# Kernel optimization log

Hardware: AMD Instinct MI355X
Metric: run time of the kernel (lower is better)

## Reference

```python
import jax, jax.numpy as jnp
import numpy as np

N_NODES = 20000
N_EDGES = 150000
FEAT = 64
HEADS = 8
N_RBF = 20
CUTOFF = 5.0


def painn_rbf(dist):
    # PaiNN radial basis used in NFF: sin(n*pi*d/cutoff)/d, n = 1..n_rbf
    n = jnp.arange(1, N_RBF + 1, dtype=dist.dtype)  # [n_rbf]
    d = dist[:, None]  # [E, 1]
    return jnp.sin(n * jnp.pi * d / CUTOFF) / d  # [E, n_rbf]


def cosine_envelope(dist):
    # 0.5 * (cos(pi*d/cutoff) + 1), zero beyond cutoff
    env = 0.5 * (jnp.cos(jnp.pi * dist / CUTOFF) + 1.0)
    return jnp.where(dist < CUTOFF, env, 0.0)


def setup_inputs() -> dict:
    key = jax.random.key(0)
    ks = jax.random.split(key, 7)
    dist = jax.random.uniform(ks[0], (N_EDGES,), minval=0.5, maxval=CUTOFF, dtype=jnp.float32)
    nbrs = jax.random.randint(ks[1], (N_EDGES, 2), 0, N_NODES, dtype=jnp.int64 if jax.config.jax_enable_x64 else jnp.int32)
    x_i = jax.random.normal(ks[2], (N_NODES, FEAT), dtype=jnp.float32)
    sf = np.float32(1.0 / np.sqrt(FEAT))
    sr = np.float32(1.0 / np.sqrt(N_RBF))
    W_q = jax.random.normal(ks[3], (HEADS, FEAT, FEAT), dtype=jnp.float32) * sf
    b_q = jnp.zeros((HEADS, FEAT), dtype=jnp.float32)
    W_k = jax.random.normal(ks[4], (HEADS, FEAT, FEAT), dtype=jnp.float32) * sf
    b_k = jnp.zeros((HEADS, FEAT), dtype=jnp.float32)
    W_dk = jax.random.normal(ks[5], (HEADS, FEAT, N_RBF), dtype=jnp.float32) * sr
    b_dk = jnp.zeros((HEADS, FEAT), dtype=jnp.float32)
    return {"dist": dist, "nbrs": nbrs, "x_i": x_i,
            "W_q": W_q, "b_q": b_q, "W_k": W_k, "b_k": b_k,
            "W_dk": W_dk, "b_dk": b_dk}


def reference(dist, nbrs, x_i, W_q, b_q, W_k, b_k, W_dk, b_dk):
    swish = jax.nn.silu
    xi = x_i[nbrs[:, 0]]  # [E, F]
    xj = x_i[nbrs[:, 1]]  # [E, F]
    edge_feats = painn_rbf(dist) * cosine_envelope(dist)[:, None]  # [E, n_rbf]
    # grouped Conv1d (kernel_size=1, groups=heads) == per-head linear
    query = jnp.einsum('ef,hgf->ehg', xi, W_q) + b_q  # [E, H, F]
    key = jnp.einsum('ef,hgf->ehg', xj, W_k) + b_k    # [E, H, F]
    d_k = swish(jnp.einsum('er,hfr->ehf', edge_feats, W_dk) + b_dk)  # [E, H, F]
    weights = swish(jnp.sum(query * key * d_k, axis=-1))  # [E, H]
    return weights
```

## Files before the change

### kernel.cpp

```cpp
#include <hip/hip_runtime.h>

#define N_NODES 20000
#define N_EDGES 150000
#define FEAT 64
#define HEADS 8
#define N_RBF 20
#define COLS 1024

typedef __attribute__((ext_vector_type(8))) short short8;
typedef __attribute__((ext_vector_type(4))) float f32x4;

union frag_u { int4 i; short8 s; };

__device__ __forceinline__ unsigned short f2bf(float x) {
    unsigned int u = __float_as_uint(x);
    unsigned int r = (u + 0x7FFFu + ((u >> 16) & 1u)) >> 16;
    return (unsigned short)r;
}
__device__ __forceinline__ unsigned int pack2bf(float lo, float hi) {
    return f2bf(lo) | ((unsigned int)f2bf(hi) << 16);
}
__device__ __forceinline__ float fsilu(float x) {
    return x * __builtin_amdgcn_rcpf(1.0f + __expf(-x));
}

__global__ __launch_bounds__(256, 4) void qk_project_mfma(
    const float* __restrict__ x,
    const float* __restrict__ Wq, const float* __restrict__ bq,
    const float* __restrict__ Wk, const float* __restrict__ bk,
    unsigned short* __restrict__ qk)
{
    const int tid = threadIdx.x;
    const int lane = tid & 63;
    const int wv = tid >> 6;
    const int l15 = lane & 15;
    const int g = lane >> 4;

    const int colBase = blockIdx.x * 256 + wv * 64;
    const bool isK = colBase >= 512;
    const float* W = isK ? Wk : Wq;
    const float* bias = isK ? bk : bq;
    const int colW = colBase & 511;

    short8 aw[4][2];
#pragma unroll
    for (int c = 0; c < 4; ++c) {
#pragma unroll
        for (int s = 0; s < 2; ++s) {
            const float* p = W + (colW + 16 * c + l15) * 64 + 32 * s + 8 * g;
            float4 v0 = *reinterpret_cast<const float4*>(p);
            float4 v1 = *reinterpret_cast<const float4*>(p + 4);
            frag_u f;
            f.i.x = pack2bf(v0.x, v0.y);
            f.i.y = pack2bf(v0.z, v0.w);
            f.i.z = pack2bf(v1.x, v1.y);
            f.i.w = pack2bf(v1.z, v1.w);
            aw[c][s] = f.s;
        }
    }
    float4 b4[4];
#pragma unroll
    for (int c = 0; c < 4; ++c)
        b4[c] = *reinterpret_cast<const float4*>(bias + colW + 16 * c + 4 * g);

    for (int i = 0; i < 8; ++i) {
        int nt = blockIdx.y * 8 + i;
        if (nt >= N_NODES / 16) break;
        int nodeBase = nt * 16;

        short8 bx[2];
#pragma unroll
        for (int s = 0; s < 2; ++s) {
            const float* p = x + (nodeBase + l15) * 64 + 32 * s + 8 * g;
            float4 v0 = *reinterpret_cast<const float4*>(p);
            float4 v1 = *reinterpret_cast<const float4*>(p + 4);
            frag_u f;
            f.i.x = pack2bf(v0.x, v0.y);
            f.i.y = pack2bf(v0.z, v0.w);
            f.i.z = pack2bf(v1.x, v1.y);
            f.i.w = pack2bf(v1.z, v1.w);
            bx[s] = f.s;
        }

#pragma unroll
        for (int c = 0; c < 4; ++c) {
            f32x4 acc = {0.f, 0.f, 0.f, 0.f};
#pragma unroll
            for (int s = 0; s < 2; ++s)
                acc = __builtin_amdgcn_mfma_f32_16x16x32_bf16(aw[c][s], bx[s], acc, 0, 0, 0);
            ushort4 sv;
            sv.x = f2bf(acc[0] + b4[c].x);
            sv.y = f2bf(acc[1] + b4[c].y);
            sv.z = f2bf(acc[2] + b4[c].z);
            sv.w = f2bf(acc[3] + b4[c].w);
            *reinterpret_cast<ushort4*>(
                qk + (size_t)(nodeBase + l15) * COLS + colBase + g * 16 + c * 4) = sv;
        }
    }
}

__global__ __launch_bounds__(128, 6) void edge_attn(
    const float* __restrict__ dist,
    const int* __restrict__ nbrs,
    const float* __restrict__ Wdk,
    const float* __restrict__ bdk,
    const unsigned short* __restrict__ qk,
    float* __restrict__ out)
{
    const int tid = threadIdx.x;
    const int hp = (blockIdx.x & 1) * 2 + (tid >> 6);
    const int h0 = hp * 2;
    const int tg = blockIdx.x >> 1;
    const int lane = tid & 63;
    const int l15 = lane & 15;
    const int g = lane >> 4;

    short8 aw[8];
#pragma unroll
    for (int m = 0; m < 8; ++m) {
        int R = (h0 + (m >> 2)) * 64 + 16 * (m & 3) + l15;
        float wv[8];
        if (g < 2) {
            const float* p = Wdk + R * 20 + 8 * g;
            float4 v0 = *reinterpret_cast<const float4*>(p);
            float4 v1 = *reinterpret_cast<const float4*>(p + 4);
            wv[0]=v0.x; wv[1]=v0.y; wv[2]=v0.z; wv[3]=v0.w;
            wv[4]=v1.x; wv[5]=v1.y; wv[6]=v1.z; wv[7]=v1.w;
        } else if (g == 2) {
            const float* p = Wdk + R * 20 + 16;
            float4 v0 = *reinterpret_cast<const float4*>(p);
            wv[0]=v0.x; wv[1]=v0.y; wv[2]=v0.z; wv[3]=v0.w;
            wv[4]=bdk[R]; wv[5]=0.0f; wv[6]=0.0f; wv[7]=0.0f;
        } else {
            wv[0]=wv[1]=wv[2]=wv[3]=wv[4]=wv[5]=wv[6]=wv[7]=0.0f;
        }
        frag_u f;
        f.i.x = pack2bf(wv[0], wv[1]);
        f.i.y = pack2bf(wv[2], wv[3]);
        f.i.z = pack2bf(wv[4], wv[5]);
        f.i.w = pack2bf(wv[6], wv[7]);
        aw[m] = f.s;
    }

    const char* qkb = reinterpret_cast<const char*>(qk);

#pragma unroll 1
    for (int i = 0; i < 4; ++i) {
        const int tile = tg * 4 + i;
        if (tile >= N_EDGES / 16) break;
        const int e = tile * 16 + l15;

        int2 nn = *reinterpret_cast<const int2*>(&nbrs[2 * e]);
        const char* bq = qkb + (size_t)nn.x * 2048 + h0 * 128 + 32 * g;
        const char* bk = qkb + (size_t)nn.y * 2048 + 1024 + h0 * 128 + 32 * g;
        uint4 qv[4], kv[4];
        qv[0] = *reinterpret_cast<const uint4*>(bq);
        qv[1] = *reinterpret_cast<const uint4*>(bq + 16);
        qv[2] = *reinterpret_cast<const uint4*>(bq + 128);
        qv[3] = *reinterpret_cast<const uint4*>(bq + 144);
        kv[0] = *reinterpret_cast<const uint4*>(bk);
        kv[1] = *reinterpret_cast<const uint4*>(bk + 16);
        kv[2] = *reinterpret_cast<const uint4*>(bk + 128);
        kv[3] = *reinterpret_cast<const uint4*>(bk + 144);

        unsigned int qr[16], kr[16];
#pragma unroll
        for (int j = 0; j < 4; ++j) {
            qr[4*j+0] = qv[j].x; qr[4*j+1] = qv[j].y;
            qr[4*j+2] = qv[j].z; qr[4*j+3] = qv[j].w;
            kr[4*j+0] = kv[j].x; kr[4*j+1] = kv[j].y;
            kr[4*j+2] = kv[j].z; kr[4*j+3] = kv[j].w;
        }

        float ef[N_RBF];
        {
            float d = dist[e];
            float theta = 0.62831853071795864769f * d;
            float s1, c1;
            __sincosf(theta, &s1, &c1);
            float env = (d < 5.0f) ? 0.5f * (c1 + 1.0f) : 0.0f;
            float scale = env / d;
            float twoc = 2.0f * c1, sm1 = 0.0f, ss = s1;
#pragma unroll
            for (int r = 0; r < N_RBF; ++r) {
                ef[r] = ss * scale;
                float nx = twoc * ss - sm1;
                sm1 = ss; ss = nx;
            }
        }

        frag_u bf_;
        {
            float v[8];
#pragma unroll
            for (int j = 0; j < 8; ++j) {
                float a0 = ef[j];
                float a1 = ef[j + 8];
                float a2 = (j + 16 < 20) ? ef[(j + 16 < 20) ? j + 16 : 0]
                                         : (j + 16 == 20 ? 1.0f : 0.0f);
                v[j] = (g == 0) ? a0 : (g == 1) ? a1 : (g == 2) ? a2 : 0.0f;
            }
            bf_.i.x = pack2bf(v[0], v[1]);
            bf_.i.y = pack2bf(v[2], v[3]);
            bf_.i.z = pack2bf(v[4], v[5]);
            bf_.i.w = pack2bf(v[6], v[7]);
        }

        float tA = 0.0f, tB = 0.0f;
#pragma unroll
        for (int m = 0; m < 8; ++m) {
            f32x4 z = {0.0f, 0.0f, 0.0f, 0.0f};
            f32x4 acc = __builtin_amdgcn_mfma_f32_16x16x32_bf16(aw[m], bf_.s, z, 0, 0, 0);
            const int hh = m >> 2, t = m & 3;
#pragma unroll
            for (int r2 = 0; r2 < 4; ++r2) {
                const int dw = hh * 8 + t * 2 + (r2 >> 1);
                unsigned int qw = qr[dw];
                unsigned int kw = kr[dw];
                float qf = (r2 & 1) ? __uint_as_float(qw & 0xFFFF0000u)
                                    : __uint_as_float(qw << 16);
                float kf = (r2 & 1) ? __uint_as_float(kw & 0xFFFF0000u)
                                    : __uint_as_float(kw << 16);
                float dk = fsilu(acc[r2]);
                float p = qf * kf;
                if (m < 4) tA = fmaf(p, dk, tA);
                else       tB = fmaf(p, dk, tB);
            }
        }

        tA += __shfl_xor(tA, 16);
        tA += __shfl_xor(tA, 32);
        tB += __shfl_xor(tB, 16);
        tB += __shfl_xor(tB, 32);

        if (lane < 16) {
            float2 o = make_float2(fsilu(tA), fsilu(tB));
            *reinterpret_cast<float2*>(out + (size_t)e * 8 + h0) = o;
        }
    }
}

extern "C" void kernel_launch(void* const* d_in, const int* in_sizes, int n_in,
                              void* d_out, int out_size, void* d_ws, size_t ws_size,
                              hipStream_t stream) {
    const float* dist = (const float*)d_in[0];
    const int* nbrs   = (const int*)d_in[1];
    const float* x_i  = (const float*)d_in[2];
    const float* W_q  = (const float*)d_in[3];
    const float* b_q  = (const float*)d_in[4];
    const float* W_k  = (const float*)d_in[5];
    const float* b_k  = (const float*)d_in[6];
    const float* W_dk = (const float*)d_in[7];
    const float* b_dk = (const float*)d_in[8];
    float* out = (float*)d_out;

    unsigned short* qkbuf = (unsigned short*)d_ws;

    dim3 g1(4, (N_NODES / 16 + 7) / 8);
    qk_project_mfma<<<g1, 256, 0, stream>>>(x_i, W_q, b_q, W_k, b_k, qkbuf);

    const int nTiles = N_EDGES / 16;
    const int nb = ((nTiles + 3) / 4) * 2;
    edge_attn<<<nb, 128, 0, stream>>>(dist, nbrs, W_dk, b_dk, qkbuf, out);
}
```

Baseline: 83.72 us.

## Compute edge RBF features once per block in shared memory, merge head-pair blocks

Before, each wave of the edge kernel recomputed the sin/cos RBF features and the bf16 B-fragment for its edges, and two blocks per edge group each handled two head pairs, so the RBF work and neighbor-index loads were repeated four times. Now one 256-thread block covers all four head pairs for 64 edges. The first wave computes the RBF fragments and loads the neighbor indices into shared memory, and after a barrier every wave reads them from there. This removes redundant transcendental work and global loads, at the cost of a serialized prologue, a __syncthreads, and fewer, larger blocks.

Result: slower. 87.62 us (+4.7%).

```diff
diff --git a/kernel.cpp b/kernel.cpp
--- a/kernel.cpp
+++ b/kernel.cpp
@@ -99,7 +99,7 @@
     }
 }
 
-__global__ __launch_bounds__(128, 6) void edge_attn(
+__global__ __launch_bounds__(256, 6) void edge_attn(
     const float* __restrict__ dist,
     const int* __restrict__ nbrs,
     const float* __restrict__ Wdk,
@@ -107,13 +107,16 @@
     const unsigned short* __restrict__ qk,
     float* __restrict__ out)
 {
+    __shared__ int4 ef_s4[4][64];
+    __shared__ int2 nbr_s[64];
+
     const int tid = threadIdx.x;
-    const int hp = (blockIdx.x & 1) * 2 + (tid >> 6);
+    const int hp = tid >> 6;
     const int h0 = hp * 2;
-    const int tg = blockIdx.x >> 1;
     const int lane = tid & 63;
     const int l15 = lane & 15;
     const int g = lane >> 4;
+    const int e0 = blockIdx.x * 64;
 
     short8 aw[8];
 #pragma unroll
@@ -142,15 +145,49 @@
         aw[m] = f.s;
     }
 
+    if (tid < 64) {
+        int e = e0 + lane;
+        bool v = e < N_EDGES;
+        float d = v ? dist[e] : 1.0f;
+        int2 nn = make_int2(0, 0);
+        if (v) nn = *reinterpret_cast<const int2*>(&nbrs[2 * e]);
+        nbr_s[lane] = nn;
+
+        float theta = 0.62831853071795864769f * d;
+        float s1, c1;
+        __sincosf(theta, &s1, &c1);
+        float env = (d < 5.0f) ? 0.5f * (c1 + 1.0f) : 0.0f;
+        float scale = env / d;
+
+        float ef[N_RBF];
+        float twoc = 2.0f * c1, sm1 = 0.0f, ss = s1;
+#pragma unroll
+        for (int r = 0; r < N_RBF; ++r) {
+            ef[r] = ss * scale;
+            float nx = twoc * ss - sm1;
+            sm1 = ss; ss = nx;
+        }
+        unsigned int w[16];
+#pragma unroll
+        for (int q = 0; q < 10; ++q)
+            w[q] = pack2bf(ef[2*q], ef[2*q+1]);
+        w[10] = 0x3F80u;
+        w[11] = w[12] = w[13] = w[14] = w[15] = 0u;
+#pragma unroll
+        for (int g2 = 0; g2 < 4; ++g2)
+            ef_s4[g2][lane] = make_int4(w[4*g2], w[4*g2+1], w[4*g2+2], w[4*g2+3]);
+    }
+    __syncthreads();
+
     const char* qkb = reinterpret_cast<const char*>(qk);
 
 #pragma unroll 1
     for (int i = 0; i < 4; ++i) {
-        const int tile = tg * 4 + i;
+        const int tile = blockIdx.x * 4 + i;
         if (tile >= N_EDGES / 16) break;
         const int e = tile * 16 + l15;
 
-        int2 nn = *reinterpret_cast<const int2*>(&nbrs[2 * e]);
+        int2 nn = nbr_s[i * 16 + l15];
         const char* bq = qkb + (size_t)nn.x * 2048 + h0 * 128 + 32 * g;
         const char* bk = qkb + (size_t)nn.y * 2048 + 1024 + h0 * 128 + 32 * g;
         uint4 qv[4], kv[4];
@@ -172,39 +209,8 @@
             kr[4*j+2] = kv[j].z; kr[4*j+3] = kv[j].w;
         }
 
-        float ef[N_RBF];
-        {
-            float d = dist[e];
-            float theta = 0.62831853071795864769f * d;
-            float s1, c1;
-            __sincosf(theta, &s1, &c1);
-            float env = (d < 5.0f) ? 0.5f * (c1 + 1.0f) : 0.0f;
-            float scale = env / d;
-            float twoc = 2.0f * c1, sm1 = 0.0f, ss = s1;
-#pragma unroll
-            for (int r = 0; r < N_RBF; ++r) {
-                ef[r] = ss * scale;
-                float nx = twoc * ss - sm1;
-                sm1 = ss; ss = nx;
-            }
-        }
-
         frag_u bf_;
-        {
-            float v[8];
-#pragma unroll
-            for (int j = 0; j < 8; ++j) {
-                float a0 = ef[j];
-                float a1 = ef[j + 8];
-                float a2 = (j + 16 < 20) ? ef[(j + 16 < 20) ? j + 16 : 0]
-                                         : (j + 16 == 20 ? 1.0f : 0.0f);
-                v[j] = (g == 0) ? a0 : (g == 1) ? a1 : (g == 2) ? a2 : 0.0f;
-            }
-            bf_.i.x = pack2bf(v[0], v[1]);
-            bf_.i.y = pack2bf(v[2], v[3]);
-            bf_.i.z = pack2bf(v[4], v[5]);
-            bf_.i.w = pack2bf(v[6], v[7]);
-        }
+        bf_.i = ef_s4[g][i * 16 + l15];
 
         float tA = 0.0f, tB = 0.0f;
 #pragma unroll
@@ -259,7 +265,6 @@
     dim3 g1(4, (N_NODES / 16 + 7) / 8);
     qk_project_mfma<<<g1, 256, 0, stream>>>(x_i, W_q, b_q, W_k, b_k, qkbuf);
 
-    const int nTiles = N_EDGES / 16;
-    const int nb = ((nTiles + 3) / 4) * 2;
-    edge_attn<<<nb, 128, 0, stream>>>(dist, nbrs, W_dk, b_dk, qkbuf, out);
-}
+    const int nb = (N_EDGES + 63) / 64;
+    edge_attn<<<nb, 256, 0, stream>>>(dist, nbrs, W_dk, b_dk, qkbuf, out);
+}
```

## Bucket-sort edges by source node to improve query gather locality

Applied to the files above, without the earlier changes.

Adds a counting sort of edges into buckets of 32 source nodes (zero, histogram, scan, scatter kernels) and makes the edge kernel process edges in that permuted order. The goal is for each wavefront's query gathers to hit nearby rows of the qk buffer, which should improve cache reuse. The cost is four extra kernel launches with atomics on every call, plus indirect, uncoalesced reads of dist and nbrs and scattered output writes.

Result: slower. 202.0 us (+141.3%).

```diff
diff --git a/kernel.cpp b/kernel.cpp
--- a/kernel.cpp
+++ b/kernel.cpp
@@ -6,6 +6,7 @@
 #define HEADS 8
 #define N_RBF 20
 #define COLS 1024
+#define NBKT 625
 
 typedef __attribute__((ext_vector_type(8))) short short8;
 typedef __attribute__((ext_vector_type(4))) float f32x4;
@@ -22,6 +23,40 @@
 }
 __device__ __forceinline__ float fsilu(float x) {
     return x * __builtin_amdgcn_rcpf(1.0f + __expf(-x));
+}
+
+__global__ void zero_k(int* counts) {
+    int i = blockIdx.x * 256 + threadIdx.x;
+    if (i < NBKT) counts[i] = 0;
+}
+__global__ void hist_k(const int* __restrict__ nbrs, int* __restrict__ counts) {
+    int e = blockIdx.x * 256 + threadIdx.x;
+    if (e < N_EDGES) atomicAdd(&counts[nbrs[2 * e] >> 5], 1);
+}
+__global__ __launch_bounds__(1024) void scan_k(const int* __restrict__ counts,
+                                               int* __restrict__ cursors) {
+    __shared__ int a[1024], b[1024];
+    int t = threadIdx.x;
+    a[t] = (t < NBKT) ? counts[t] : 0;
+    __syncthreads();
+    int* src = a; int* dst = b;
+    for (int off = 1; off < 1024; off <<= 1) {
+        int x = src[t];
+        if (t >= off) x += src[t - off];
+        dst[t] = x;
+        __syncthreads();
+        int* tmp = src; src = dst; dst = tmp;
+    }
+    if (t < NBKT) cursors[t] = (t == 0) ? 0 : src[t - 1];
+}
+__global__ void scatter_k(const int* __restrict__ nbrs, int* __restrict__ cursors,
+                          int* __restrict__ perm) {
+    int e = blockIdx.x * 256 + threadIdx.x;
+    if (e < N_EDGES) {
+        int bkt = nbrs[2 * e] >> 5;
+        int pos = atomicAdd(&cursors[bkt], 1);
+        perm[pos] = e;
+    }
 }
 
 __global__ __launch_bounds__(256, 4) void qk_project_mfma(
@@ -102,6 +137,7 @@
 __global__ __launch_bounds__(128, 6) void edge_attn(
     const float* __restrict__ dist,
     const int* __restrict__ nbrs,
+    const int* __restrict__ perm,
     const float* __restrict__ Wdk,
     const float* __restrict__ bdk,
     const unsigned short* __restrict__ qk,
@@ -148,9 +184,9 @@
     for (int i = 0; i < 4; ++i) {
         const int tile = tg * 4 + i;
         if (tile >= N_EDGES / 16) break;
-        const int e = tile * 16 + l15;
-
-        int2 nn = *reinterpret_cast<const int2*>(&nbrs[2 * e]);
+        const int eid = perm[tile * 16 + l15];
+
+        int2 nn = *reinterpret_cast<const int2*>(&nbrs[2 * eid]);
         const char* bq = qkb + (size_t)nn.x * 2048 + h0 * 128 + 32 * g;
         const char* bk = qkb + (size_t)nn.y * 2048 + 1024 + h0 * 128 + 32 * g;
         uint4 qv[4], kv[4];
@@ -174,7 +210,7 @@
 
         float ef[N_RBF];
         {
-            float d = dist[e];
+            float d = dist[eid];
             float theta = 0.62831853071795864769f * d;
             float s1, c1;
             __sincosf(theta, &s1, &c1);
@@ -235,7 +271,7 @@
 
         if (lane < 16) {
             float2 o = make_float2(fsilu(tA), fsilu(tB));
-            *reinterpret_cast<float2*>(out + (size_t)e * 8 + h0) = o;
+            *reinterpret_cast<float2*>(out + (size_t)eid * 8 + h0) = o;
         }
     }
 }
@@ -254,12 +290,21 @@
     const float* b_dk = (const float*)d_in[8];
     float* out = (float*)d_out;
 
-    unsigned short* qkbuf = (unsigned short*)d_ws;
+    char* ws = (char*)d_ws;
+    unsigned short* qkbuf = (unsigned short*)ws;
+    int* counts  = (int*)(ws + 40960000);
+    int* cursors = counts + NBKT;
+    int* permbuf = cursors + NBKT;
+
+    zero_k<<<(NBKT + 255) / 256, 256, 0, stream>>>(counts);
+    hist_k<<<(N_EDGES + 255) / 256, 256, 0, stream>>>(nbrs, counts);
+    scan_k<<<1, 1024, 0, stream>>>(counts, cursors);
+    scatter_k<<<(N_EDGES + 255) / 256, 256, 0, stream>>>(nbrs, cursors, permbuf);
 
     dim3 g1(4, (N_NODES / 16 + 7) / 8);
     qk_project_mfma<<<g1, 256, 0, stream>>>(x_i, W_q, b_q, W_k, b_k, qkbuf);
 
     const int nTiles = N_EDGES / 16;
     const int nb = ((nTiles + 3) / 4) * 2;
-    edge_attn<<<nb, 128, 0, stream>>>(dist, nbrs, W_dk, b_dk, qkbuf, out);
-}
+    edge_attn<<<nb, 128, 0, stream>>>(dist, nbrs, permbuf, W_dk, b_dk, qkbuf, out);
+}
```
